# Kernel tuning notes

Measured on AMD Instinct MI355X. Metric: run time of the kernel, lower is better.

## Reference

```python
import jax, jax.numpy as jnp
import numpy as np


def _log_exp_kernel(x):
    # positive feature map log(1 + exp(x)) (softplus), per the kernel's name
    return jax.nn.softplus(x)


def setup_inputs() -> dict:
    key0 = jax.random.key(0)
    ks = jax.random.split(key0, 8)
    N, L, H, d = 2, 2048, 8, 64
    D = H * d
    s = 1.0 / np.sqrt(D)
    return {
        "query": jax.random.normal(ks[0], (N, L, D), jnp.float32),
        "key": jax.random.normal(ks[1], (N, L, D), jnp.float32),
        "Wq": jax.random.normal(ks[2], (D, D), jnp.float32) * s,
        "Wk": jax.random.normal(ks[3], (D, D), jnp.float32) * s,
        "Wv": jax.random.normal(ks[4], (D, D), jnp.float32) * s,
        "position_coeffs": jax.random.normal(ks[5], (H, d), jnp.float32),
        "position_weight": jax.random.normal(ks[6], (H, d, 1), jnp.float32) * 0.02,
        "position_bias": jax.random.normal(ks[7], (H, d), jnp.float32) * 0.02,
    }


def reference(query, key, Wq, Wk, Wv, position_coeffs, position_weight, position_bias):
    N, Lq, D = query.shape
    Lk = key.shape[1]
    H, d, P = position_weight.shape

    # default positions: arange, P=1 (broadcast over batch)
    qpos = jnp.arange(Lq, dtype=query.dtype).reshape(1, Lq, 1)  # (1, Lq, P)

    # projections + kernel feature map; (N, H, L, d)
    q = _log_exp_kernel((query @ Wq.T).reshape(N, Lq, H, d)).transpose(0, 2, 1, 3)
    k = _log_exp_kernel((key @ Wk.T).reshape(N, Lk, H, d)).transpose(0, 2, 1, 3)
    v = (key @ Wv.T).reshape(N, Lk, H, d).transpose(0, 2, 1, 3)

    # projected positions; NOTE: source uses query_positions for pk too (faithful)
    pq = jnp.einsum('nlp,hkp->nhlk', qpos, position_weight) + position_bias[None, :, None, :]
    pk = jnp.einsum('nlp,hkp->nhlk', qpos, position_weight)  # (1, H, Lq, d)

    coeff = position_coeffs[None, :, None, :]  # (1, H, 1, d)
    cos_a = q * jnp.cos(pq)
    cos_b = coeff * k * jnp.cos(pk)
    sin_a = q * jnp.sin(pq)
    sin_b = coeff * k * jnp.sin(pk)

    # (N, H, Lq, Lk) quadratic score
    score = (jnp.einsum('nhqd,nhkd->nhqk', cos_a, cos_b)
             + jnp.einsum('nhqd,nhkd->nhqk', sin_a, sin_b))

    # future mask (future_offset = 0): zero out keys j > query i
    future = jnp.arange(Lk)[None, :] > jnp.arange(Lq)[:, None]
    score = jnp.where(future[None, None], jnp.zeros((), score.dtype), score)

    # scaled: rows sum (in abs) to 1
    score = score / jnp.sum(jnp.abs(score), axis=-1, keepdims=True)

    att = jnp.einsum('nhqk,nhkd->nhqd', score, v)
    return att.transpose(0, 2, 1, 3).reshape(N, Lq, D)
```

## Files before the change

### kernel.cpp

```cpp
#include <hip/hip_runtime.h>
#include <hip/hip_bf16.h>
#include <cstdint>


typedef __bf16 bf16x8 __attribute__((ext_vector_type(8)));
typedef float f32x16 __attribute__((ext_vector_type(16)));
typedef unsigned short u16x8 __attribute__((ext_vector_type(8)));
typedef uint32_t u32x4 __attribute__((ext_vector_type(4)));

__device__ __forceinline__ unsigned short f2bfu(float f) {
    uint32_t u = __float_as_uint(f);
    uint32_t r = (u + 0x7fffu + ((u >> 16) & 1u)) >> 16;
    return (unsigned short)r;
}
__device__ __forceinline__ uint32_t cvt2(float a, float b) {
    __hip_bfloat162 h = __float22bfloat162_rn(make_float2(a, b));
    return *reinterpret_cast<uint32_t*>(&h);
}
__device__ __forceinline__ float softplusf(float x) {
    return fmaxf(x, 0.f) + __logf(1.f + __expf(-fabsf(x)));
}
__device__ __forceinline__ uint32_t pkbf(float a, float b) {
    uint32_t d;
    asm("v_cvt_pk_bf16_f32 %0, %1, %2" : "=v"(d) : "v"(a), "v"(b));
    return d;
}
__device__ __forceinline__ void plswap(uint32_t& a, uint32_t& b) {
    asm volatile("v_permlane32_swap_b32 %0, %1" : "+v"(a), "+v"(b));
}

__global__ __launch_bounds__(256) void cvt_kernel(
    const float* __restrict__ query, const float* __restrict__ key,
    const float* __restrict__ Wq, const float* __restrict__ Wk,
    const float* __restrict__ Wv,
    unsigned short* __restrict__ Xqb, unsigned short* __restrict__ Xkb,
    unsigned short* __restrict__ Wqb, unsigned short* __restrict__ Wkb,
    unsigned short* __restrict__ Wvb)
{
    const int z = blockIdx.z;
    const float* src;
    unsigned short* dst;
    int n8;
    if (z == 0)      { src = query; dst = Xqb; n8 = 4096 * 512 / 8; }
    else if (z == 1) { src = key;   dst = Xkb; n8 = 4096 * 512 / 8; }
    else if (z == 2) { src = Wq;    dst = Wqb; n8 = 512 * 512 / 8;  }
    else if (z == 3) { src = Wk;    dst = Wkb; n8 = 512 * 512 / 8;  }
    else             { src = Wv;    dst = Wvb; n8 = 512 * 512 / 8;  }
    int idx = blockIdx.x * 256 + threadIdx.x;
    if (idx >= n8) return;
    const float4* s = (const float4*)src + (size_t)idx * 2;
    float4 a = s[0], b = s[1];
    uint4 o;
    o.x = cvt2(a.x, a.y); o.y = cvt2(a.z, a.w);
    o.z = cvt2(b.x, b.y); o.w = cvt2(b.z, b.w);
    *(uint4*)&dst[(size_t)idx * 8] = o;
}

__global__ __launch_bounds__(256) void proj_kernel(
    const unsigned short* __restrict__ Xqb, const unsigned short* __restrict__ Xkb,
    const unsigned short* __restrict__ Wqb, const unsigned short* __restrict__ Wkb,
    const unsigned short* __restrict__ Wvb, const float* __restrict__ coef,
    const float* __restrict__ posw, const float* __restrict__ posb,
    unsigned short* __restrict__ Af, unsigned short* __restrict__ Bf,
    unsigned short* __restrict__ Vf)
{
    const int mode = blockIdx.z;
    const int c0 = blockIdx.x * 64;
    const int m0 = blockIdx.y * 128;
    const unsigned short* X = (mode == 0) ? Xqb : Xkb;
    const unsigned short* W = (mode == 0) ? Wqb : (mode == 1 ? Wkb : Wvb);

    __shared__ __align__(16) char smem[(128 + 64) * 72 * 2];
    unsigned short* Xs = (unsigned short*)smem;
    unsigned short* Ws = (unsigned short*)(smem + 128 * 72 * 2);

    const int t = threadIdx.x;
    const int lane = t & 63, wv = t >> 6;
    const int lm = lane & 31, half = lane >> 5;
    const int wrow = wv >> 1, wcol = wv & 1;

    f32x16 acc[2] = {};

    u16x8 px[4], pw[2];
    {
#pragma unroll
        for (int it = 0; it < 4; ++it) {
            int cid = t + it * 256, row = cid >> 3, seg = cid & 7;
            px[it] = *(const u16x8*)&X[(size_t)(m0 + row) * 512 + seg * 8];
        }
#pragma unroll
        for (int it = 0; it < 2; ++it) {
            int cid = t + it * 256, row = cid >> 3, seg = cid & 7;
            pw[it] = *(const u16x8*)&W[(size_t)(c0 + row) * 512 + seg * 8];
        }
    }

    for (int kt = 0; kt < 8; ++kt) {
        __syncthreads();
#pragma unroll
        for (int it = 0; it < 4; ++it) {
            int cid = t + it * 256, row = cid >> 3, seg = cid & 7;
            *(u16x8*)&Xs[row * 72 + seg * 8] = px[it];
        }
#pragma unroll
        for (int it = 0; it < 2; ++it) {
            int cid = t + it * 256, row = cid >> 3, seg = cid & 7;
            *(u16x8*)&Ws[row * 72 + seg * 8] = pw[it];
        }
        __syncthreads();
        if (kt < 7) {
            int ko = (kt + 1) * 64;
#pragma unroll
            for (int it = 0; it < 4; ++it) {
                int cid = t + it * 256, row = cid >> 3, seg = cid & 7;
                px[it] = *(const u16x8*)&X[(size_t)(m0 + row) * 512 + ko + seg * 8];
            }
#pragma unroll
            for (int it = 0; it < 2; ++it) {
                int cid = t + it * 256, row = cid >> 3, seg = cid & 7;
                pw[it] = *(const u16x8*)&W[(size_t)(c0 + row) * 512 + ko + seg * 8];
            }
        }
        const unsigned short* ab = &Xs[(64 * wrow + lm) * 72 + half * 8];
        const unsigned short* bb = &Ws[(32 * wcol + lm) * 72 + half * 8];
        __builtin_amdgcn_s_setprio(1);
#pragma unroll
        for (int ks = 0; ks < 4; ++ks) {
            bf16x8 a0 = *(const bf16x8*)(ab + ks * 16);
            bf16x8 a1 = *(const bf16x8*)(ab + 32 * 72 + ks * 16);
            bf16x8 b  = *(const bf16x8*)(bb + ks * 16);
            acc[0] = __builtin_amdgcn_mfma_f32_32x32x16_bf16(a0, b, acc[0], 0, 0, 0);
            acc[1] = __builtin_amdgcn_mfma_f32_32x32x16_bf16(a1, b, acc[1], 0, 0, 0);
        }
        __builtin_amdgcn_s_setprio(0);
    }

    if (mode != 2) {
        unsigned short* Feat = (mode == 0) ? Af : Bf;
        int c = c0 + 32 * wcol + lm;
        int h = c >> 6, jj = c & 63;
        float wgt = posw[c];
        float bia = (mode == 0) ? posb[c] : 0.f;
        float cf  = (mode == 1) ? coef[c] : 1.f;
#pragma unroll
        for (int i = 0; i < 2; ++i)
#pragma unroll
        for (int r = 0; r < 16; ++r) {
            int rl = (r & 3) + 8 * (r >> 2) + 4 * half;
            int m = m0 + 64 * wrow + 32 * i + rl;
            int n = m >> 11, l = m & 2047;
            float ang = (float)l * wgt + bia;
            float sn, cs; __sincosf(ang, &sn, &cs);
            float v = softplusf(acc[i][r]) * cf;
            size_t base = ((size_t)(n * 8 + h) * 2048 + l) * 128 + jj;
            Feat[base]      = f2bfu(v * cs);
            Feat[base + 64] = f2bfu(v * sn);
        }
    } else {
        float* tb = (float*)smem;
        float* tbw = tb + wv * (32 * 34);
        __syncthreads();
#pragma unroll
        for (int i = 0; i < 2; ++i) {
#pragma unroll
            for (int r = 0; r < 16; ++r) {
                int rl = (r & 3) + 8 * (r >> 2) + 4 * half;
                tbw[lm * 34 + rl] = acc[i][r];
            }
            int mb = m0 + 64 * wrow + 32 * i;
            int n = mb >> 11, l0 = mb & 2047;
#pragma unroll
            for (int rep = 0; rep < 16; ++rep) {
                int cl = rep * 2 + half;
                float v = tbw[cl * 34 + lm];
                int c = c0 + 32 * wcol + cl;
                int h = c >> 6, dd = c & 63;
                Vf[((size_t)(n * 8 + h) * 64 + dd) * 2048 + l0 + lm] = f2bfu(v);
            }
        }
    }
}

__global__ __launch_bounds__(256) void attn_kernel(
    const unsigned short* __restrict__ Af, const unsigned short* __restrict__ Bf,
    const unsigned short* __restrict__ Vf, float* __restrict__ out)
{
    const int bx = blockIdx.x;
    const int nh = bx & 15;
    const int p  = bx >> 4;
    const int qq = (p < 16) ? p : 47 - p;
    const int q0 = qq * 64;

    __shared__ unsigned short Bs[64 * 136];
    __shared__ unsigned short Vs[64 * 72];
    __shared__ float zf[64];

    const int t = threadIdx.x;
    const int lane = t & 63, wv = t >> 6;
    const int lm = lane & 31, half = lane >> 5;
    const int qb = wv >> 1, kb = wv & 1;
    const int n = nh >> 3, h = nh & 7;

    const unsigned short* Ah = Af + (size_t)nh * 2048 * 128;
    const unsigned short* Bh = Bf + (size_t)nh * 2048 * 128;
    const unsigned short* Vh = Vf + (size_t)nh * 64 * 2048;

#pragma unroll
    for (int it = 0; it < 4; ++it) {
        int cid = t + it * 256, row = cid >> 4, off = (cid & 15) << 3;
        *(u16x8*)&Bs[row * 136 + off] = *(const u16x8*)&Ah[(size_t)(q0 + row) * 128 + off];
    }
    if (t < 64) zf[t] = 0.f;
    __syncthreads();
    bf16x8 qfrag[8];
    {
        const unsigned short* ab = &Bs[(32 * qb + lm) * 136 + half * 8];
#pragma unroll
        for (int c = 0; c < 8; ++c) qfrag[c] = *(const bf16x8*)(ab + c * 16);
    }

    f32x16 oacc0 = {}, oacc1 = {};
    float zsum = 0.f;

    u16x8 pb[4], pv[2];
#pragma unroll
    for (int it = 0; it < 4; ++it) {
        int cid = t + it * 256, row = cid >> 4, off = (cid & 15) << 3;
        pb[it] = *(const u16x8*)&Bh[(size_t)row * 128 + off];
    }
#pragma unroll
    for (int it = 0; it < 2; ++it) {
        int cid = t + it * 256, row = cid >> 3, off = (cid & 7) << 3;
        pv[it] = *(const u16x8*)&Vh[(size_t)row * 2048 + off];
    }

    for (int kt = 0; kt <= qq; ++kt) {
        __syncthreads();
#pragma unroll
        for (int it = 0; it < 4; ++it) {
            int cid = t + it * 256, row = cid >> 4, off = (cid & 15) << 3;
            *(u16x8*)&Bs[row * 136 + off] = pb[it];
        }
#pragma unroll
        for (int it = 0; it < 2; ++it) {
            int cid = t + it * 256, row = cid >> 3, off = (cid & 7) << 3;
            *(u16x8*)&Vs[row * 72 + off] = pv[it];
        }
        __syncthreads();
        if (kt < qq) {
            int k1 = (kt + 1) * 64;
#pragma unroll
            for (int it = 0; it < 4; ++it) {
                int cid = t + it * 256, row = cid >> 4, off = (cid & 15) << 3;
                pb[it] = *(const u16x8*)&Bh[(size_t)(k1 + row) * 128 + off];
            }
#pragma unroll
            for (int it = 0; it < 2; ++it) {
                int cid = t + it * 256, row = cid >> 3, off = (cid & 7) << 3;
                pv[it] = *(const u16x8*)&Vh[(size_t)row * 2048 + k1 + off];
            }
        }

        f32x16 sacc = {};
        const unsigned short* kbase = &Bs[(32 * kb + lm) * 136 + half * 8];
        __builtin_amdgcn_s_setprio(1);
#pragma unroll
        for (int ks = 0; ks < 8; ++ks) {
            bf16x8 kf = *(const bf16x8*)(kbase + ks * 16);
            sacc = __builtin_amdgcn_mfma_f32_32x32x16_bf16(kf, qfrag[ks], sacc, 0, 0, 0);
        }
        __builtin_amdgcn_s_setprio(0);

        if (kt == qq) {
#pragma unroll
            for (int r = 0; r < 16; ++r) {
                int kl = (r & 3) + 8 * (r >> 2) + 4 * half;
                if ((32 * kb + kl) > (32 * qb + lm)) sacc[r] = 0.f;
            }
        }
#pragma unroll
        for (int r = 0; r < 16; ++r) zsum += fabsf(sacc[r]);

        union { u32x4 u; bf16x8 b; } pa0, pa1;
        {
            uint32_t A = pkbf(sacc[0], sacc[1]);
            uint32_t B = pkbf(sacc[2], sacc[3]);
            uint32_t C = pkbf(sacc[4], sacc[5]);
            uint32_t D = pkbf(sacc[6], sacc[7]);
            plswap(A, C);
            plswap(B, D);
            pa0.u = (u32x4){A, B, C, D};
            uint32_t E = pkbf(sacc[8], sacc[9]);
            uint32_t F = pkbf(sacc[10], sacc[11]);
            uint32_t G = pkbf(sacc[12], sacc[13]);
            uint32_t H = pkbf(sacc[14], sacc[15]);
            plswap(E, G);
            plswap(F, H);
            pa1.u = (u32x4){E, F, G, H};
        }

        const unsigned short* v0 = &Vs[(size_t)lm * 72 + 32 * kb + half * 8];
        const unsigned short* v1 = &Vs[(size_t)(32 + lm) * 72 + 32 * kb + half * 8];
        __builtin_amdgcn_s_setprio(1);
        {
            bf16x8 vb00 = *(const bf16x8*)(v0);
            bf16x8 vb10 = *(const bf16x8*)(v1);
            oacc0 = __builtin_amdgcn_mfma_f32_32x32x16_bf16(pa0.b, vb00, oacc0, 0, 0, 0);
            oacc1 = __builtin_amdgcn_mfma_f32_32x32x16_bf16(pa0.b, vb10, oacc1, 0, 0, 0);
            bf16x8 vb01 = *(const bf16x8*)(v0 + 16);
            bf16x8 vb11 = *(const bf16x8*)(v1 + 16);
            oacc0 = __builtin_amdgcn_mfma_f32_32x32x16_bf16(pa1.b, vb01, oacc0, 0, 0, 0);
            oacc1 = __builtin_amdgcn_mfma_f32_32x32x16_bf16(pa1.b, vb11, oacc1, 0, 0, 0);
        }
        __builtin_amdgcn_s_setprio(0);
    }

    atomicAdd(&zf[32 * qb + lm], zsum);
    __syncthreads();

    float* Os = (float*)Bs;
    if (kb == 0) {
#pragma unroll
        for (int r = 0; r < 16; ++r) {
            int ql = (r & 3) + 8 * (r >> 2) + 4 * half;
            Os[(32 * qb + ql) * 65 + lm]      = oacc0[r];
            Os[(32 * qb + ql) * 65 + 32 + lm] = oacc1[r];
        }
    }
    __syncthreads();
    if (kb == 1) {
#pragma unroll
        for (int r = 0; r < 16; ++r) {
            int ql = (r & 3) + 8 * (r >> 2) + 4 * half;
            int q = q0 + 32 * qb + ql;
            float invz = 1.f / zf[32 * qb + ql];
            float o0 = (Os[(32 * qb + ql) * 65 + lm]      + oacc0[r]) * invz;
            float o1 = (Os[(32 * qb + ql) * 65 + 32 + lm] + oacc1[r]) * invz;
            size_t base = ((size_t)(n * 2048 + q)) * 512 + h * 64;
            out[base + lm]      = o0;
            out[base + 32 + lm] = o1;
        }
    }
}

extern "C" void kernel_launch(void* const* d_in, const int* in_sizes, int n_in,
                              void* d_out, int out_size, void* d_ws, size_t ws_size,
                              hipStream_t stream) {
    (void)in_sizes; (void)n_in; (void)out_size; (void)ws_size;
    const float* query = (const float*)d_in[0];
    const float* key   = (const float*)d_in[1];
    const float* Wq    = (const float*)d_in[2];
    const float* Wk    = (const float*)d_in[3];
    const float* Wv    = (const float*)d_in[4];
    const float* coef  = (const float*)d_in[5];
    const float* posw  = (const float*)d_in[6];
    const float* posb  = (const float*)d_in[7];

    unsigned short* Af  = (unsigned short*)d_ws;
    unsigned short* Bf  = Af + (size_t)16 * 2048 * 128;
    unsigned short* Vf  = Bf + (size_t)16 * 2048 * 128;
    unsigned short* Xqb = Vf + (size_t)16 * 64 * 2048;
    unsigned short* Xkb = Xqb + (size_t)4096 * 512;
    unsigned short* Wqb = Xkb + (size_t)4096 * 512;
    unsigned short* Wkb = Wqb + (size_t)512 * 512;
    unsigned short* Wvb = Wkb + (size_t)512 * 512;

    cvt_kernel<<<dim3(1024, 1, 5), 256, 0, stream>>>(
        query, key, Wq, Wk, Wv, Xqb, Xkb, Wqb, Wkb, Wvb);
    proj_kernel<<<dim3(8, 32, 3), 256, 0, stream>>>(
        Xqb, Xkb, Wqb, Wkb, Wvb, coef, posw, posb, Af, Bf, Vf);
    attn_kernel<<<dim3(512), 256, 0, stream>>>(
        Af, Bf, Vf, (float*)d_out);
}
```

Measured before the change: 128.3 us.

## Double-buffer K/V shared tiles, split QK accumulators, schedule longest tiles first

Double-buffers the K and V shared-memory tiles so each iteration needs one barrier instead of two. The QK^T MFMA chain is split into two independent accumulators that are summed afterwards, which shortens the dependency chain. Block ordering changes from a paired load-balance mapping to longest-row-first (qq descending). The extra buffers double LDS use, which may lower occupancy. Correctness depends on one barrier per iteration being enough to protect the alternating buffers.

After: 130.2 us. About the same (+1.5%).

```diff
diff --git a/kernel.cpp b/kernel.cpp
--- a/kernel.cpp
+++ b/kernel.cpp
@@ -187,12 +187,11 @@
 {
     const int bx = blockIdx.x;
     const int nh = bx & 15;
-    const int p  = bx >> 4;
-    const int qq = (p < 16) ? p : 47 - p;
+    const int qq = 31 - (bx >> 4);
     const int q0 = qq * 64;
 
-    __shared__ unsigned short Bs[64 * 136];
-    __shared__ unsigned short Vs[64 * 72];
+    __shared__ unsigned short Bs[2][64 * 136];
+    __shared__ unsigned short Vs[2][64 * 72];
     __shared__ float zf[64];
 
     const int t = threadIdx.x;
@@ -208,16 +207,17 @@
 #pragma unroll
     for (int it = 0; it < 4; ++it) {
         int cid = t + it * 256, row = cid >> 4, off = (cid & 15) << 3;
-        *(u16x8*)&Bs[row * 136 + off] = *(const u16x8*)&Ah[(size_t)(q0 + row) * 128 + off];
+        *(u16x8*)&Bs[0][row * 136 + off] = *(const u16x8*)&Ah[(size_t)(q0 + row) * 128 + off];
     }
     if (t < 64) zf[t] = 0.f;
     __syncthreads();
     bf16x8 qfrag[8];
     {
-        const unsigned short* ab = &Bs[(32 * qb + lm) * 136 + half * 8];
+        const unsigned short* ab = &Bs[0][(32 * qb + lm) * 136 + half * 8];
 #pragma unroll
         for (int c = 0; c < 8; ++c) qfrag[c] = *(const bf16x8*)(ab + c * 16);
     }
+    __syncthreads();
 
     f32x16 oacc0 = {}, oacc1 = {};
     float zsum = 0.f;
@@ -234,19 +234,20 @@
         pv[it] = *(const u16x8*)&Vh[(size_t)row * 2048 + off];
     }
 
+    int c = 0;
     for (int kt = 0; kt <= qq; ++kt) {
-        __syncthreads();
+        unsigned short* bsc = Bs[c];
+        unsigned short* vsc = Vs[c];
 #pragma unroll
         for (int it = 0; it < 4; ++it) {
             int cid = t + it * 256, row = cid >> 4, off = (cid & 15) << 3;
-            *(u16x8*)&Bs[row * 136 + off] = pb[it];
+            *(u16x8*)&bsc[row * 136 + off] = pb[it];
         }
 #pragma unroll
         for (int it = 0; it < 2; ++it) {
             int cid = t + it * 256, row = cid >> 3, off = (cid & 7) << 3;
-            *(u16x8*)&Vs[row * 72 + off] = pv[it];
-        }
-        __syncthreads();
+            *(u16x8*)&vsc[row * 72 + off] = pv[it];
+        }
         if (kt < qq) {
             int k1 = (kt + 1) * 64;
 #pragma unroll
@@ -260,16 +261,22 @@
                 pv[it] = *(const u16x8*)&Vh[(size_t)row * 2048 + k1 + off];
             }
         }
-
-        f32x16 sacc = {};
-        const unsigned short* kbase = &Bs[(32 * kb + lm) * 136 + half * 8];
+        __syncthreads();
+
+        f32x16 sa = {}, sb = {};
+        const unsigned short* kbase = &bsc[(32 * kb + lm) * 136 + half * 8];
         __builtin_amdgcn_s_setprio(1);
 #pragma unroll
-        for (int ks = 0; ks < 8; ++ks) {
-            bf16x8 kf = *(const bf16x8*)(kbase + ks * 16);
-            sacc = __builtin_amdgcn_mfma_f32_32x32x16_bf16(kf, qfrag[ks], sacc, 0, 0, 0);
+        for (int ks = 0; ks < 4; ++ks) {
+            bf16x8 kf0 = *(const bf16x8*)(kbase + ks * 16);
+            bf16x8 kf1 = *(const bf16x8*)(kbase + (ks + 4) * 16);
+            sa = __builtin_amdgcn_mfma_f32_32x32x16_bf16(kf0, qfrag[ks],     sa, 0, 0, 0);
+            sb = __builtin_amdgcn_mfma_f32_32x32x16_bf16(kf1, qfrag[ks + 4], sb, 0, 0, 0);
         }
         __builtin_amdgcn_s_setprio(0);
+        f32x16 sacc;
+#pragma unroll
+        for (int r = 0; r < 16; ++r) sacc[r] = sa[r] + sb[r];
 
         if (kt == qq) {
 #pragma unroll
@@ -299,8 +306,8 @@
             pa1.u = (u32x4){E, F, G, H};
         }
 
-        const unsigned short* v0 = &Vs[(size_t)lm * 72 + 32 * kb + half * 8];
-        const unsigned short* v1 = &Vs[(size_t)(32 + lm) * 72 + 32 * kb + half * 8];
+        const unsigned short* v0 = &vsc[(size_t)lm * 72 + 32 * kb + half * 8];
+        const unsigned short* v1 = &vsc[(size_t)(32 + lm) * 72 + 32 * kb + half * 8];
         __builtin_amdgcn_s_setprio(1);
         {
             bf16x8 vb00 = *(const bf16x8*)(v0);
@@ -313,6 +320,7 @@
             oacc1 = __builtin_amdgcn_mfma_f32_32x32x16_bf16(pa1.b, vb11, oacc1, 0, 0, 0);
         }
         __builtin_amdgcn_s_setprio(0);
+        c ^= 1;
     }
 
     atomicAdd(&zf[32 * qb + lm], zsum);
```

## Double-buffer projection GEMM tiles via direct global-to-LDS loads with XOR swizzle

Applied to the files above, without the earlier changes.

Replaces register-staged global loads followed by LDS stores in the projection GEMM with global_load_lds direct copies into a double-buffered shared-memory tile. The tile layout changes from a padded stride to an XOR-swizzled 64-column layout to avoid bank conflicts. Explicit vmcnt waits and barriers let the next k-tile load overlap the current tile's MFMAs. It doubles LDS use and relies on hand-written waitcnt counts being correct.

Result: no change. 130.0 us (+1.3%).

```diff
diff --git a/kernel.cpp b/kernel.cpp
--- a/kernel.cpp
+++ b/kernel.cpp
@@ -27,6 +27,11 @@
 }
 __device__ __forceinline__ void plswap(uint32_t& a, uint32_t& b) {
     asm volatile("v_permlane32_swap_b32 %0, %1" : "+v"(a), "+v"(b));
+}
+__device__ __forceinline__ void gload16(const unsigned short* g, unsigned short* l) {
+    __builtin_amdgcn_global_load_lds(
+        (const __attribute__((address_space(1))) unsigned int*)g,
+        (__attribute__((address_space(3))) unsigned int*)l, 16, 0, 0);
 }
 
 __global__ __launch_bounds__(256) void cvt_kernel(
@@ -56,6 +61,9 @@
     *(uint4*)&dst[(size_t)idx * 8] = o;
 }
 
+#define XTILE (128 * 64)
+#define WTILE (64 * 64)
+
 __global__ __launch_bounds__(256) void proj_kernel(
     const unsigned short* __restrict__ Xqb, const unsigned short* __restrict__ Xkb,
     const unsigned short* __restrict__ Wqb, const unsigned short* __restrict__ Wkb,
@@ -70,9 +78,7 @@
     const unsigned short* X = (mode == 0) ? Xqb : Xkb;
     const unsigned short* W = (mode == 0) ? Wqb : (mode == 1 ? Wkb : Wvb);
 
-    __shared__ __align__(16) char smem[(128 + 64) * 72 * 2];
-    unsigned short* Xs = (unsigned short*)smem;
-    unsigned short* Ws = (unsigned short*)(smem + 128 * 72 * 2);
+    __shared__ __align__(16) unsigned short smem[2 * XTILE + 2 * WTILE];
 
     const int t = threadIdx.x;
     const int lane = t & 63, wv = t >> 6;
@@ -81,58 +87,53 @@
 
     f32x16 acc[2] = {};
 
-    u16x8 px[4], pw[2];
-    {
+    auto stage = [&](int kt, int b) {
+        int ko = kt * 64;
+        unsigned short* xd = smem + b * XTILE;
+        unsigned short* wd = smem + 2 * XTILE + b * WTILE;
 #pragma unroll
         for (int it = 0; it < 4; ++it) {
             int cid = t + it * 256, row = cid >> 3, seg = cid & 7;
-            px[it] = *(const u16x8*)&X[(size_t)(m0 + row) * 512 + seg * 8];
+            const unsigned short* src =
+                X + (size_t)(m0 + row) * 512 + ko + (((seg ^ (row & 7)) << 3));
+            gload16(src, xd + cid * 8);
         }
 #pragma unroll
         for (int it = 0; it < 2; ++it) {
             int cid = t + it * 256, row = cid >> 3, seg = cid & 7;
-            pw[it] = *(const u16x8*)&W[(size_t)(c0 + row) * 512 + seg * 8];
-        }
-    }
-
+            const unsigned short* src =
+                W + (size_t)(c0 + row) * 512 + ko + (((seg ^ (row & 7)) << 3));
+            gload16(src, wd + cid * 8);
+        }
+    };
+
+    stage(0, 0);
+    const int rx = 64 * wrow + lm, rw = 32 * wcol + lm;
     for (int kt = 0; kt < 8; ++kt) {
-        __syncthreads();
-#pragma unroll
-        for (int it = 0; it < 4; ++it) {
-            int cid = t + it * 256, row = cid >> 3, seg = cid & 7;
-            *(u16x8*)&Xs[row * 72 + seg * 8] = px[it];
-        }
-#pragma unroll
-        for (int it = 0; it < 2; ++it) {
-            int cid = t + it * 256, row = cid >> 3, seg = cid & 7;
-            *(u16x8*)&Ws[row * 72 + seg * 8] = pw[it];
-        }
-        __syncthreads();
         if (kt < 7) {
-            int ko = (kt + 1) * 64;
-#pragma unroll
-            for (int it = 0; it < 4; ++it) {
-                int cid = t + it * 256, row = cid >> 3, seg = cid & 7;
-                px[it] = *(const u16x8*)&X[(size_t)(m0 + row) * 512 + ko + seg * 8];
-            }
-#pragma unroll
-            for (int it = 0; it < 2; ++it) {
-                int cid = t + it * 256, row = cid >> 3, seg = cid & 7;
-                pw[it] = *(const u16x8*)&W[(size_t)(c0 + row) * 512 + ko + seg * 8];
-            }
-        }
-        const unsigned short* ab = &Xs[(64 * wrow + lm) * 72 + half * 8];
-        const unsigned short* bb = &Ws[(32 * wcol + lm) * 72 + half * 8];
+            stage(kt + 1, (kt + 1) & 1);
+            asm volatile("s_waitcnt vmcnt(6)" ::: "memory");
+        } else {
+            asm volatile("s_waitcnt vmcnt(0)" ::: "memory");
+        }
+        __builtin_amdgcn_s_barrier();
+
+        const unsigned short* xb = smem + (kt & 1) * XTILE;
+        const unsigned short* wb = smem + 2 * XTILE + (kt & 1) * WTILE;
         __builtin_amdgcn_s_setprio(1);
 #pragma unroll
         for (int ks = 0; ks < 4; ++ks) {
-            bf16x8 a0 = *(const bf16x8*)(ab + ks * 16);
-            bf16x8 a1 = *(const bf16x8*)(ab + 32 * 72 + ks * 16);
-            bf16x8 b  = *(const bf16x8*)(bb + ks * 16);
+            int sA = (((half + 2 * ks) ^ (lm & 7)) << 3);
+            bf16x8 a0 = *(const bf16x8*)&xb[rx * 64 + sA];
+            bf16x8 a1 = *(const bf16x8*)&xb[(rx + 32) * 64 + sA];
+            bf16x8 b  = *(const bf16x8*)&wb[rw * 64 + sA];
             acc[0] = __builtin_amdgcn_mfma_f32_32x32x16_bf16(a0, b, acc[0], 0, 0, 0);
             acc[1] = __builtin_amdgcn_mfma_f32_32x32x16_bf16(a1, b, acc[1], 0, 0, 0);
         }
         __builtin_amdgcn_s_setprio(0);
+        asm volatile("s_waitcnt lgkmcnt(0)" ::: "memory");
+        __builtin_amdgcn_sched_barrier(0);
+        __builtin_amdgcn_s_barrier();
     }
 
     if (mode != 2) {
```

## Double-buffer attention K/V tiles via direct global-to-LDS loads with XOR swizzle

Applied to the files above, without the earlier changes.

Replaces the register-staged K/V prefetch in the attention kernel with asynchronous global_load_lds copies into double-buffered LDS, synchronised with explicit vmcnt waits and raw barriers. The padded LDS layout becomes an XOR-swizzled unpadded layout to avoid bank conflicts, and Q fragments are read straight from global memory instead of through LDS. This aims to cut register pressure and the LDS-store/sync overhead per tile, at the cost of more LDS and delicate hand-written waitcnt ordering.

After: 133.8 us. 1.04x slower.

```diff
diff --git a/kernel.cpp b/kernel.cpp
--- a/kernel.cpp
+++ b/kernel.cpp
@@ -27,6 +27,11 @@
 }
 __device__ __forceinline__ void plswap(uint32_t& a, uint32_t& b) {
     asm volatile("v_permlane32_swap_b32 %0, %1" : "+v"(a), "+v"(b));
+}
+__device__ __forceinline__ void gload16(const unsigned short* g, unsigned short* l) {
+    __builtin_amdgcn_global_load_lds(
+        (const __attribute__((address_space(1))) unsigned int*)g,
+        (__attribute__((address_space(3))) unsigned int*)l, 16, 0, 0);
 }
 
 __global__ __launch_bounds__(256) void cvt_kernel(
@@ -191,8 +196,8 @@
     const int qq = (p < 16) ? p : 47 - p;
     const int q0 = qq * 64;
 
-    __shared__ unsigned short Bs[64 * 136];
-    __shared__ unsigned short Vs[64 * 72];
+    __shared__ __align__(16) unsigned short Bsm[2 * 64 * 128];
+    __shared__ __align__(16) unsigned short Vsm[2 * 64 * 64];
     __shared__ float zf[64];
 
     const int t = threadIdx.x;
@@ -205,68 +210,57 @@
     const unsigned short* Bh = Bf + (size_t)nh * 2048 * 128;
     const unsigned short* Vh = Vf + (size_t)nh * 64 * 2048;
 
-#pragma unroll
-    for (int it = 0; it < 4; ++it) {
-        int cid = t + it * 256, row = cid >> 4, off = (cid & 15) << 3;
-        *(u16x8*)&Bs[row * 136 + off] = *(const u16x8*)&Ah[(size_t)(q0 + row) * 128 + off];
-    }
-    if (t < 64) zf[t] = 0.f;
-    __syncthreads();
     bf16x8 qfrag[8];
     {
-        const unsigned short* ab = &Bs[(32 * qb + lm) * 136 + half * 8];
-#pragma unroll
-        for (int c = 0; c < 8; ++c) qfrag[c] = *(const bf16x8*)(ab + c * 16);
-    }
+        const unsigned short* qr = &Ah[(size_t)(q0 + 32 * qb + lm) * 128 + half * 8];
+#pragma unroll
+        for (int c = 0; c < 8; ++c) qfrag[c] = *(const bf16x8*)(qr + c * 16);
+    }
+    if (t < 64) zf[t] = 0.f;
 
     f32x16 oacc0 = {}, oacc1 = {};
     float zsum = 0.f;
 
-    u16x8 pb[4], pv[2];
-#pragma unroll
-    for (int it = 0; it < 4; ++it) {
-        int cid = t + it * 256, row = cid >> 4, off = (cid & 15) << 3;
-        pb[it] = *(const u16x8*)&Bh[(size_t)row * 128 + off];
-    }
-#pragma unroll
-    for (int it = 0; it < 2; ++it) {
-        int cid = t + it * 256, row = cid >> 3, off = (cid & 7) << 3;
-        pv[it] = *(const u16x8*)&Vh[(size_t)row * 2048 + off];
-    }
+    auto stage = [&](int kt, int b) {
+        const int k0 = kt * 64;
+        unsigned short* bd = Bsm + b * (64 * 128);
+        unsigned short* vd = Vsm + b * (64 * 64);
+#pragma unroll
+        for (int it = 0; it < 4; ++it) {
+            int cid = t + it * 256, row = cid >> 4, sd = cid & 15;
+            gload16(&Bh[(size_t)(k0 + row) * 128 + ((sd ^ (row & 15)) << 3)],
+                    bd + cid * 8);
+        }
+#pragma unroll
+        for (int it = 0; it < 2; ++it) {
+            int cid = t + it * 256, row = cid >> 3, sd = cid & 7;
+            gload16(&Vh[(size_t)row * 2048 + k0 + ((sd ^ (row & 7)) << 3)],
+                    vd + cid * 8);
+        }
+    };
+
+    stage(0, 0);
+    const int krow = 32 * kb + lm;
+    const int xm16 = lm & 15, xm8 = lm & 7;
 
     for (int kt = 0; kt <= qq; ++kt) {
-        __syncthreads();
-#pragma unroll
-        for (int it = 0; it < 4; ++it) {
-            int cid = t + it * 256, row = cid >> 4, off = (cid & 15) << 3;
-            *(u16x8*)&Bs[row * 136 + off] = pb[it];
-        }
-#pragma unroll
-        for (int it = 0; it < 2; ++it) {
-            int cid = t + it * 256, row = cid >> 3, off = (cid & 7) << 3;
-            *(u16x8*)&Vs[row * 72 + off] = pv[it];
-        }
-        __syncthreads();
         if (kt < qq) {
-            int k1 = (kt + 1) * 64;
-#pragma unroll
-            for (int it = 0; it < 4; ++it) {
-                int cid = t + it * 256, row = cid >> 4, off = (cid & 15) << 3;
-                pb[it] = *(const u16x8*)&Bh[(size_t)(k1 + row) * 128 + off];
-            }
-#pragma unroll
-            for (int it = 0; it < 2; ++it) {
-                int cid = t + it * 256, row = cid >> 3, off = (cid & 7) << 3;
-                pv[it] = *(const u16x8*)&Vh[(size_t)row * 2048 + k1 + off];
-            }
-        }
+            stage(kt + 1, (kt + 1) & 1);
+            asm volatile("s_waitcnt vmcnt(6)" ::: "memory");
+        } else {
+            asm volatile("s_waitcnt vmcnt(0)" ::: "memory");
+        }
+        __builtin_amdgcn_s_barrier();
+
+        const unsigned short* bsrc = Bsm + (kt & 1) * (64 * 128);
+        const unsigned short* vsrc = Vsm + (kt & 1) * (64 * 64);
 
         f32x16 sacc = {};
-        const unsigned short* kbase = &Bs[(32 * kb + lm) * 136 + half * 8];
         __builtin_amdgcn_s_setprio(1);
 #pragma unroll
         for (int ks = 0; ks < 8; ++ks) {
-            bf16x8 kf = *(const bf16x8*)(kbase + ks * 16);
+            int s = (((ks * 2 + half) ^ xm16) << 3);
+            bf16x8 kf = *(const bf16x8*)&bsrc[krow * 128 + s];
             sacc = __builtin_amdgcn_mfma_f32_32x32x16_bf16(kf, qfrag[ks], sacc, 0, 0, 0);
         }
         __builtin_amdgcn_s_setprio(0);
@@ -299,26 +293,28 @@
             pa1.u = (u32x4){E, F, G, H};
         }
 
-        const unsigned short* v0 = &Vs[(size_t)lm * 72 + 32 * kb + half * 8];
-        const unsigned short* v1 = &Vs[(size_t)(32 + lm) * 72 + 32 * kb + half * 8];
+        int s00 = (((4 * kb + half) ^ xm8) << 3);
+        int s01 = (((4 * kb + half + 2) ^ xm8) << 3);
+        bf16x8 vb00 = *(const bf16x8*)&vsrc[lm * 64 + s00];
+        bf16x8 vb01 = *(const bf16x8*)&vsrc[lm * 64 + s01];
+        bf16x8 vb10 = *(const bf16x8*)&vsrc[(32 + lm) * 64 + s00];
+        bf16x8 vb11 = *(const bf16x8*)&vsrc[(32 + lm) * 64 + s01];
         __builtin_amdgcn_s_setprio(1);
-        {
-            bf16x8 vb00 = *(const bf16x8*)(v0);
-            bf16x8 vb10 = *(const bf16x8*)(v1);
-            oacc0 = __builtin_amdgcn_mfma_f32_32x32x16_bf16(pa0.b, vb00, oacc0, 0, 0, 0);
-            oacc1 = __builtin_amdgcn_mfma_f32_32x32x16_bf16(pa0.b, vb10, oacc1, 0, 0, 0);
-            bf16x8 vb01 = *(const bf16x8*)(v0 + 16);
-            bf16x8 vb11 = *(const bf16x8*)(v1 + 16);
-            oacc0 = __builtin_amdgcn_mfma_f32_32x32x16_bf16(pa1.b, vb01, oacc0, 0, 0, 0);
-            oacc1 = __builtin_amdgcn_mfma_f32_32x32x16_bf16(pa1.b, vb11, oacc1, 0, 0, 0);
-        }
+        oacc0 = __builtin_amdgcn_mfma_f32_32x32x16_bf16(pa0.b, vb00, oacc0, 0, 0, 0);
+        oacc1 = __builtin_amdgcn_mfma_f32_32x32x16_bf16(pa0.b, vb10, oacc1, 0, 0, 0);
+        oacc0 = __builtin_amdgcn_mfma_f32_32x32x16_bf16(pa1.b, vb01, oacc0, 0, 0, 0);
+        oacc1 = __builtin_amdgcn_mfma_f32_32x32x16_bf16(pa1.b, vb11, oacc1, 0, 0, 0);
         __builtin_amdgcn_s_setprio(0);
+
+        asm volatile("s_waitcnt lgkmcnt(0)" ::: "memory");
+        __builtin_amdgcn_sched_barrier(0);
+        __builtin_amdgcn_s_barrier();
     }
 
     atomicAdd(&zf[32 * qb + lm], zsum);
     __syncthreads();
 
-    float* Os = (float*)Bs;
+    float* Os = (float*)Bsm;
     if (kb == 0) {
 #pragma unroll
         for (int r = 0; r < 16; ++r) {
```
